# Optimization experiments

Hardware: AMD Instinct MI355X
Metric: run time of the kernel (lower is better)

Reference implementation:

```python
import jax, jax.numpy as jnp
import numpy as np

D_MODEL = 1024
D_KV = 64
N_HEADS = 16
INNER = N_HEADS * D_KV
EPS = 1e-6


def setup_inputs() -> dict:
    key = jax.random.key(0)
    ks = jax.random.split(key, 8)
    B, SQ, SKV = 2, 2048, 4096
    hidden_states = jax.random.normal(ks[0], (B, SQ, D_MODEL), dtype=jnp.float32)
    key_value_states = jax.random.normal(ks[1], (B, SKV, D_MODEL), dtype=jnp.float32)
    attention_mask = jnp.zeros((B, 1, 1, SKV), dtype=jnp.float32)
    # nn.Linear(in, out, bias=False): y = x @ W.T; store W as [in, out] here
    s = 0.02
    Wq = jax.random.normal(ks[2], (D_MODEL, INNER), dtype=jnp.float32) * s
    Wk = jax.random.normal(ks[3], (D_MODEL, INNER), dtype=jnp.float32) * s
    Wv = jax.random.normal(ks[4], (D_MODEL, INNER), dtype=jnp.float32) * s
    Wo = jax.random.normal(ks[5], (INNER, D_MODEL), dtype=jnp.float32) * s
    ln_weight = jnp.ones((D_MODEL,), dtype=jnp.float32)
    return {
        "hidden_states": hidden_states,
        "key_value_states": key_value_states,
        "attention_mask": attention_mask,
        "ln_weight": ln_weight,
        "Wq": Wq,
        "Wk": Wk,
        "Wv": Wv,
        "Wo": Wo,
    }


def _t5_rmsnorm(x, w, eps=EPS):
    # no mean subtraction, variance in fp32
    var = jnp.mean(jnp.square(x.astype(jnp.float32)), axis=-1, keepdims=True)
    return w * (x * jax.lax.rsqrt(var + eps)).astype(x.dtype)


def reference(hidden_states, key_value_states, attention_mask, ln_weight, Wq, Wk, Wv, Wo):
    B, SQ, _ = hidden_states.shape
    SKV = key_value_states.shape[1]
    normed = _t5_rmsnorm(hidden_states, ln_weight)

    # projections -> [B, H, S, Dk]
    q = (normed @ Wq).reshape(B, SQ, N_HEADS, D_KV).transpose(0, 2, 1, 3)
    k = (key_value_states @ Wk).reshape(B, SKV, N_HEADS, D_KV).transpose(0, 2, 1, 3)
    v = (key_value_states @ Wv).reshape(B, SKV, N_HEADS, D_KV).transpose(0, 2, 1, 3)

    # T5: NO 1/sqrt(d) scaling
    scores = jnp.einsum("bhqd,bhkd->bhqk", q, k) + attention_mask
    attn = jax.nn.softmax(scores.astype(jnp.float32), axis=-1).astype(scores.dtype)
    ctx = jnp.einsum("bhqk,bhkd->bhqd", attn, v)
    ctx = ctx.transpose(0, 2, 1, 3).reshape(B, SQ, INNER)
    attn_out = ctx @ Wo
    return hidden_states + attn_out
```

## Files before the change

kernel.cpp:

```cpp
#include <hip/hip_runtime.h>

typedef unsigned short u16;
typedef unsigned int u32;
typedef __attribute__((ext_vector_type(4))) float f32x4;
typedef __attribute__((ext_vector_type(8))) short short8;
typedef __attribute__((ext_vector_type(4))) short short4v;

#define BB   2
#define SQL  2048
#define SKVL 4096
#define DM   1024
#define NH   16
#define DK   64
#define L2E  1.44269504f

#if __has_builtin(__builtin_amdgcn_exp2f)
#define EXP2(x) __builtin_amdgcn_exp2f(x)
#else
#define EXP2(x) exp2f(x)
#endif

#define MFMA32(a, b, c) __builtin_amdgcn_mfma_f32_16x16x32_bf16(a, b, c, 0, 0, 0)

__device__ __forceinline__ u16 f2bf(float f) {
  union { float f; unsigned u; } v; v.f = f;
  unsigned r = v.u + 0x7fff + ((v.u >> 16) & 1);
  return (u16)(r >> 16);
}

__device__ __forceinline__ short4v pack4(float p0, float p1, float p2, float p3) {
  union { float f; u32 u; } a, b, c, d;
  a.f = p0; b.f = p1; c.f = p2; d.f = p3;
  union { uint2 v; short4v s; } r;
  r.v.x = __builtin_amdgcn_perm(b.u + 0x8000u, a.u + 0x8000u, 0x07060302);
  r.v.y = __builtin_amdgcn_perm(d.u + 0x8000u, c.u + 0x8000u, 0x07060302);
  return r.s;
}

__device__ __forceinline__ void gload16(const void* g, void* lds) {
  __builtin_amdgcn_global_load_lds(
      (const __attribute__((address_space(1))) unsigned int*)g,
      (__attribute__((address_space(3))) unsigned int*)lds, 16, 0, 0);
}

__global__ void pre_kernel(const float* __restrict__ hidden, const float* __restrict__ lnw,
                           const float* __restrict__ kvs,
                           const float* __restrict__ Wq, const float* __restrict__ Wk,
                           const float* __restrict__ Wv, const float* __restrict__ Wo,
                           u16* __restrict__ normed, u16* __restrict__ kvb,
                           u16* __restrict__ Wqt, u16* __restrict__ Wkt,
                           u16* __restrict__ Wvt, u16* __restrict__ Wot) {
  __shared__ float red[4];
  __shared__ float tile[32][33];
  int bid = blockIdx.x, t = threadIdx.x;
  if (bid < 4096) {
    int row = bid;
    float4 v = ((const float4*)(hidden + (size_t)row * DM))[t];
    float ss = v.x * v.x + v.y * v.y + v.z * v.z + v.w * v.w;
#pragma unroll
    for (int m = 32; m >= 1; m >>= 1) ss += __shfl_xor(ss, m, 64);
    int lane = t & 63, wv = t >> 6;
    if (lane == 0) red[wv] = ss;
    __syncthreads();
    float total = red[0] + red[1] + red[2] + red[3];
    float scale = rsqrtf(total * (1.0f / DM) + 1e-6f);
    float4 g = ((const float4*)lnw)[t];
    ushort4 o;
    o.x = f2bf(v.x * scale * g.x);
    o.y = f2bf(v.y * scale * g.y);
    o.z = f2bf(v.z * scale * g.z);
    o.w = f2bf(v.w * scale * g.w);
    ((ushort4*)(normed + (size_t)row * DM))[t] = o;
  } else if (bid < 12288) {
    int i = (bid - 4096) * 256 + t;
    float4 v = ((const float4*)kvs)[i];
    ushort4 o;
    o.x = f2bf(v.x); o.y = f2bf(v.y); o.z = f2bf(v.z); o.w = f2bf(v.w);
    ((ushort4*)kvb)[i] = o;
  } else {
    int g = bid - 12288;
    int z = g >> 10;
    const float* W = (z == 0) ? Wq : (z == 1) ? Wk : (z == 2) ? Wv : Wo;
    u16* Wt = (z == 0) ? Wqt : (z == 1) ? Wkt : (z == 2) ? Wvt : Wot;
    int xx = g & 31, yy = (g >> 5) & 31;
    int tx = t & 31, ty = t >> 5;
    int k0 = yy * 32, n0 = xx * 32;
#pragma unroll
    for (int i = 0; i < 4; i++)
      tile[ty + i * 8][tx] = W[(size_t)(k0 + ty + i * 8) * DM + n0 + tx];
    __syncthreads();
#pragma unroll
    for (int i = 0; i < 4; i++)
      Wt[(size_t)(n0 + ty + i * 8) * DM + k0 + tx] = f2bf(tile[tx][ty + i * 8]);
  }
}

__global__ __launch_bounds__(512, 1) void proj_kernel(
    const u16* __restrict__ normed, const u16* __restrict__ kvb,
    const u16* __restrict__ Wqt, const u16* __restrict__ Wkt,
    const u16* __restrict__ Wvt,
    u16* __restrict__ Qb, u16* __restrict__ Kbf, u16* __restrict__ Vtb) {
  const int K = 1024;
  __shared__ __align__(16) u16 Al[256 * 32];
  __shared__ __align__(16) u16 B1[128 * 32];
  __shared__ __align__(16) u16 B2[128 * 32];
  int tid = threadIdx.x, lane = tid & 63, w = tid >> 6;
  int l15 = lane & 15, quad = lane >> 4;
  int wy = w >> 1, wx = w & 1;
  int bid = blockIdx.x;

  if (bid < 256) {
    int tm = (bid >> 3) * 256, tn = (bid & 7) * 128;
    f32x4 ak[4][4] = {}, av[4][4] = {};
    for (int k0 = 0; k0 < K; k0 += 32) {
      __syncthreads();
#pragma unroll
      for (int r = 0; r < 2; r++) {
        int mg = w * 2 + r;
        gload16(kvb + (size_t)(tm + mg * 16 + l15) * K + k0 + quad * 8, &Al[mg * 512]);
      }
      gload16(Wkt + (size_t)(tn + w * 16 + l15) * K + k0 + quad * 8, &B1[w * 512]);
      gload16(Wvt + (size_t)(tn + w * 16 + l15) * K + k0 + quad * 8, &B2[w * 512]);
      __syncthreads();
      short8 af[4], bk[4], bv[4];
#pragma unroll
      for (int i = 0; i < 4; i++) {
        af[i] = *(const short8*)&Al[((wy * 4 + i) * 64 + lane) * 8];
        bk[i] = *(const short8*)&B1[((wx * 4 + i) * 64 + lane) * 8];
        bv[i] = *(const short8*)&B2[((wx * 4 + i) * 64 + lane) * 8];
      }
#pragma unroll
      for (int mt = 0; mt < 4; mt++)
#pragma unroll
        for (int nt = 0; nt < 4; nt++) {
          ak[mt][nt] = MFMA32(af[mt], bk[nt], ak[mt][nt]);
          av[mt][nt] = MFMA32(af[mt], bv[nt], av[mt][nt]);
        }
    }
#pragma unroll
    for (int mt = 0; mt < 4; mt++) {
      int m0 = tm + wy * 64 + mt * 16 + quad * 4;
      int bB = m0 >> 12, skv0 = m0 & 4095;
      int t32 = skv0 >> 5, p0 = skv0 & 31;
#pragma unroll
      for (int nt = 0; nt < 4; nt++) {
        int n = tn + wx * 64 + nt * 16 + l15;
        int h = n >> 6, d0 = n & 63;
        size_t vbase = ((size_t)((bB * NH + h) * 128 + t32)) * 2048
                     + (size_t)(d0 >> 4) * 512 + (size_t)(d0 & 15) * 8;
#pragma unroll
        for (int r = 0; r < 4; r++) {
          Kbf[(size_t)(m0 + r) * 1024 + n] = f2bf(ak[mt][nt][r]);
          int p = p0 + r;
          int s = ((p >> 2) & 3) * 8 + ((p >> 4) & 1) * 4 + (p & 3);
          Vtb[vbase + (s >> 3) * 128 + (s & 7)] = f2bf(av[mt][nt][r]);
        }
      }
    }
  } else {
    int qid = bid - 256;
    int tm = (qid >> 3) * 128, tn = (qid & 7) * 128;
    f32x4 acc[2][4] = {};
    for (int k0 = 0; k0 < K; k0 += 32) {
      __syncthreads();
      gload16(normed + (size_t)(tm + w * 16 + l15) * K + k0 + quad * 8, &Al[w * 512]);
      gload16(Wqt + (size_t)(tn + w * 16 + l15) * K + k0 + quad * 8, &B1[w * 512]);
      __syncthreads();
      short8 af[2], bfr[4];
#pragma unroll
      for (int i = 0; i < 2; i++)
        af[i] = *(const short8*)&Al[((wy * 2 + i) * 64 + lane) * 8];
#pragma unroll
      for (int i = 0; i < 4; i++)
        bfr[i] = *(const short8*)&B1[((wx * 4 + i) * 64 + lane) * 8];
#pragma unroll
      for (int mt = 0; mt < 2; mt++)
#pragma unroll
        for (int nt = 0; nt < 4; nt++)
          acc[mt][nt] = MFMA32(af[mt], bfr[nt], acc[mt][nt]);
    }
#pragma unroll
    for (int mt = 0; mt < 2; mt++) {
      int m0 = tm + wy * 32 + mt * 16 + quad * 4;
#pragma unroll
      for (int nt = 0; nt < 4; nt++) {
        int n = tn + wx * 64 + nt * 16 + l15;
#pragma unroll
        for (int r = 0; r < 4; r++)
          Qb[(size_t)(m0 + r) * 1024 + n] = f2bf(acc[mt][nt][r] * L2E);
      }
    }
  }
}

__global__ __launch_bounds__(256, 2) void flash_kernel(
    const u16* __restrict__ Qp, const u16* __restrict__ Kp, const u16* __restrict__ Vtb,
    const float* __restrict__ mask, u16* __restrict__ ctx) {
  __shared__ __align__(16) char smem[65536];
  u16* Kbuf = (u16*)smem;
  u16* Vbuf = (u16*)(smem + 32768);
  float* Ox = (float*)smem;
  float* Ll = (float*)(smem + 32768);

  int tid = threadIdx.x, lane = tid & 63, w = tid >> 6;
  int l15 = lane & 15, quad = lane >> 4;
  int grp = w >> 1, wg = w & 1;

  int lid = blockIdx.y * 16 + blockIdx.x;
  int xcd = lid & 7, slot = lid >> 3;
  int bh = xcd * 4 + (slot >> 4);
  int qb = slot & 15;
  int b = bh >> 4, h = bh & 15;
  int q0 = qb * 128 + wg * 64;

  short8 qf[4][2];
#pragma unroll
  for (int mt = 0; mt < 4; mt++)
#pragma unroll
    for (int kf = 0; kf < 2; kf++)
      qf[mt][kf] = *(const short8*)(Qp + (size_t)(b * SQL + q0 + mt * 16 + l15) * DM +
                                    h * DK + kf * 32 + quad * 8);

  f32x4 of[4][4] = {};
  f32x4 la[4] = {};
  const short8 ones8 = {0x3F80, 0x3F80, 0x3F80, 0x3F80, 0x3F80, 0x3F80, 0x3F80, 0x3F80};

  const size_t vblob = (size_t)(b * NH + h) * 262144;
  const float* mrow = mask + (size_t)b * SKVL;

  auto stage = [&](int tileIdx, int buf) {
    int kv0 = tileIdx * 64;
    u16* Kd = Kbuf + (buf * 2 + grp) * 4096;
    u16* Vd = Vbuf + (buf * 2 + grp) * 4096;
#pragma unroll
    for (int r = 0; r < 4; r++) {
      int u = wg * 4 + r;
      int kt = u >> 1, kf = u & 1;
      gload16(Kp + (size_t)(b * SKVL + kv0 + kt * 16 + l15) * DM + h * DK + kf * 32 + quad * 8,
              &Kd[u * 512]);
      gload16(Vtb + vblob + (size_t)tileIdx * 4096 + u * 512 + lane * 8, &Vd[u * 512]);
    }
  };

  f32x4 mlc[4], mln[4];
  {
    int kv0 = grp * 64;
#pragma unroll
    for (int kt = 0; kt < 4; kt++)
      mlc[kt] = *(const f32x4*)(mrow + kv0 + kt * 16 + quad * 4) * L2E;
  }
  stage(grp, 0);

  union PU { short8 v8; short4v h2[2]; };

  for (int it = 0; it < 32; ++it) {
    __syncthreads();
    if (it + 1 < 32) {
      stage((it + 1) * 2 + grp, (it + 1) & 1);
      int kvn = ((it + 1) * 2 + grp) * 64;
#pragma unroll
      for (int kt = 0; kt < 4; kt++)
        mln[kt] = *(const f32x4*)(mrow + kvn + kt * 16 + quad * 4) * L2E;
    }
    const u16* Kg = Kbuf + ((it & 1) * 2 + grp) * 4096;
    const u16* Vg = Vbuf + ((it & 1) * 2 + grp) * 4096;

    __builtin_amdgcn_s_setprio(1);
#pragma unroll
    for (int ktp = 0; ktp < 2; ktp++) {
      PU paf[4];
#pragma unroll
      for (int kth = 0; kth < 2; kth++) {
        int kt = ktp * 2 + kth;
        short8 k0 = *(const short8*)&Kg[((kt * 2 + 0) * 64 + lane) * 8];
        short8 k1 = *(const short8*)&Kg[((kt * 2 + 1) * 64 + lane) * 8];
#pragma unroll
        for (int mt = 0; mt < 4; mt++) {
          f32x4 st = mlc[kt];
          st = MFMA32(k0, qf[mt][0], st);
          st = MFMA32(k1, qf[mt][1], st);
          paf[mt].h2[kth] = pack4(EXP2(st[0]), EXP2(st[1]), EXP2(st[2]), EXP2(st[3]));
        }
      }
#pragma unroll
      for (int mt = 0; mt < 4; mt++)
        la[mt] = MFMA32(paf[mt].v8, ones8, la[mt]);
#pragma unroll
      for (int nt = 0; nt < 4; nt++) {
        short8 vv = *(const short8*)&Vg[ktp * 2048 + (nt * 64 + lane) * 8];
#pragma unroll
        for (int mt = 0; mt < 4; mt++)
          of[mt][nt] = MFMA32(paf[mt].v8, vv, of[mt][nt]);
      }
    }
    __builtin_amdgcn_s_setprio(0);
#pragma unroll
    for (int kt = 0; kt < 4; kt++) mlc[kt] = mln[kt];
  }

  __syncthreads();
  if (grp == 1) {
#pragma unroll
    for (int mt = 0; mt < 4; mt++) {
#pragma unroll
      for (int nt = 0; nt < 4; nt++)
#pragma unroll
        for (int r = 0; r < 4; r++)
          Ox[(wg * 64 + mt * 16 + quad * 4 + r) * 64 + nt * 16 + l15] = of[mt][nt][r];
      if (l15 == 0)
#pragma unroll
        for (int r = 0; r < 4; r++) Ll[wg * 64 + mt * 16 + quad * 4 + r] = la[mt][r];
    }
  }
  __syncthreads();
  if (grp == 0) {
#pragma unroll
    for (int mt = 0; mt < 4; mt++)
#pragma unroll
      for (int r = 0; r < 4; r++) {
        int ql = wg * 64 + mt * 16 + quad * 4 + r;
        float inv = 1.0f / (la[mt][r] + Ll[ql]);
        int q = qb * 128 + ql;
#pragma unroll
        for (int nt = 0; nt < 4; nt++) {
          float ov = of[mt][nt][r] + Ox[ql * 64 + nt * 16 + l15];
          ctx[(size_t)(b * SQL + q) * DM + h * DK + nt * 16 + l15] = f2bf(ov * inv);
        }
      }
  }
}

__global__ void ogemm_kernel(const u16* __restrict__ A, const u16* __restrict__ Bt,
                             float* __restrict__ C, const float* __restrict__ resid) {
  const int K = 1024;
  __shared__ __align__(16) u16 Al[128 * 32];
  __shared__ __align__(16) u16 Bl[128 * 32];
  int tid = threadIdx.x, lane = tid & 63, w = tid >> 6;
  int l15 = lane & 15, quad = lane >> 4;
  int wy = w >> 1, wx = w & 1;
  int tm = blockIdx.x * 128, tn = blockIdx.y * 128;
  f32x4 acc[4][4] = {};

  for (int k0 = 0; k0 < K; k0 += 32) {
    __syncthreads();
#pragma unroll
    for (int r = 0; r < 2; r++) {
      int mg = w * 2 + r;
      gload16(A + (size_t)(tm + mg * 16 + l15) * K + k0 + quad * 8, &Al[mg * 512]);
      gload16(Bt + (size_t)(tn + mg * 16 + l15) * K + k0 + quad * 8, &Bl[mg * 512]);
    }
    __syncthreads();
    short8 af[4], bfr[4];
#pragma unroll
    for (int i = 0; i < 4; i++) {
      af[i] = *(const short8*)&Al[((wy * 4 + i) * 64 + lane) * 8];
      bfr[i] = *(const short8*)&Bl[((wx * 4 + i) * 64 + lane) * 8];
    }
#pragma unroll
    for (int mt = 0; mt < 4; mt++)
#pragma unroll
      for (int nt = 0; nt < 4; nt++)
        acc[mt][nt] = MFMA32(af[mt], bfr[nt], acc[mt][nt]);
  }

#pragma unroll
  for (int mt = 0; mt < 4; mt++) {
    int m0 = tm + wy * 64 + mt * 16 + quad * 4;
#pragma unroll
    for (int nt = 0; nt < 4; nt++) {
      int n = tn + wx * 64 + nt * 16 + l15;
#pragma unroll
      for (int r = 0; r < 4; r++) {
        size_t idx = (size_t)(m0 + r) * 1024 + n;
        C[idx] = resid[idx] + acc[mt][nt][r];
      }
    }
  }
}

extern "C" void kernel_launch(void* const* d_in, const int* in_sizes, int n_in,
                              void* d_out, int out_size, void* d_ws, size_t ws_size,
                              hipStream_t stream) {
  const float* hidden = (const float*)d_in[0];
  const float* kvs    = (const float*)d_in[1];
  const float* mask   = (const float*)d_in[2];
  const float* lnw    = (const float*)d_in[3];
  const float* Wq     = (const float*)d_in[4];
  const float* Wk     = (const float*)d_in[5];
  const float* Wv     = (const float*)d_in[6];
  const float* Wo     = (const float*)d_in[7];
  char* ws = (char*)d_ws;

  u16* normed = (u16*)(ws + 0);
  u16* kvb    = (u16*)(ws + 8388608);
  u16* Wqt    = (u16*)(ws + 25165824);
  u16* Wkt    = (u16*)(ws + 27262976);
  u16* Wvt    = (u16*)(ws + 29360128);
  u16* Wot    = (u16*)(ws + 31457280);
  u16* Qb     = (u16*)(ws + 33554432);
  u16* Kbf    = (u16*)(ws + 41943040);
  u16* Vtb    = (u16*)(ws + 58720256);
  u16* ctxb   = (u16*)(ws + 75497472);

  pre_kernel<<<16384, 256, 0, stream>>>(hidden, lnw, kvs, Wq, Wk, Wv, Wo,
                                        normed, kvb, Wqt, Wkt, Wvt, Wot);
  proj_kernel<<<512, 512, 0, stream>>>(normed, kvb, Wqt, Wkt, Wvt, Qb, Kbf, Vtb);
  flash_kernel<<<dim3(SQL / 128, BB * NH), 256, 0, stream>>>(Qb, Kbf, Vtb, mask, ctxb);
  ogemm_kernel<<<dim3(32, 8), 256, 0, stream>>>(ctxb, Wot, (float*)d_out, hidden);
}
```

Measured before the change: 310.4 us.

## Double-buffer LDS in projection GEMM and shrink output GEMM tiles

The projection kernel now keeps two LDS buffers and prefetches the next K-slice while the current one feeds the MFMAs, which removes one barrier per iteration and overlaps global loads with compute. Its launch bounds are raised to allow two blocks per CU. The output GEMM tile shrinks from 128x128 to 64x64, so the grid grows from 256 to 1024 blocks and fills more CUs. The cost is double the LDS use in the projection kernel, possible register pressure from the occupancy hint, and less data reuse per block in the output GEMM.

```diff
diff --git a/kernel.cpp b/kernel.cpp
--- a/kernel.cpp
+++ b/kernel.cpp
@@ -95,15 +95,15 @@
   }
 }
 
-__global__ __launch_bounds__(512, 1) void proj_kernel(
+__global__ __launch_bounds__(512, 2) void proj_kernel(
     const u16* __restrict__ normed, const u16* __restrict__ kvb,
     const u16* __restrict__ Wqt, const u16* __restrict__ Wkt,
     const u16* __restrict__ Wvt,
     u16* __restrict__ Qb, u16* __restrict__ Kbf, u16* __restrict__ Vtb) {
   const int K = 1024;
-  __shared__ __align__(16) u16 Al[256 * 32];
-  __shared__ __align__(16) u16 B1[128 * 32];
-  __shared__ __align__(16) u16 B2[128 * 32];
+  __shared__ __align__(16) u16 Al[2][256 * 32];
+  __shared__ __align__(16) u16 B1[2][128 * 32];
+  __shared__ __align__(16) u16 B2[2][128 * 32];
   int tid = threadIdx.x, lane = tid & 63, w = tid >> 6;
   int l15 = lane & 15, quad = lane >> 4;
   int wy = w >> 1, wx = w & 1;
@@ -112,22 +112,28 @@
   if (bid < 256) {
     int tm = (bid >> 3) * 256, tn = (bid & 7) * 128;
     f32x4 ak[4][4] = {}, av[4][4] = {};
-    for (int k0 = 0; k0 < K; k0 += 32) {
-      __syncthreads();
+
+    auto stage = [&](int k0, int buf) {
 #pragma unroll
       for (int r = 0; r < 2; r++) {
         int mg = w * 2 + r;
-        gload16(kvb + (size_t)(tm + mg * 16 + l15) * K + k0 + quad * 8, &Al[mg * 512]);
-      }
-      gload16(Wkt + (size_t)(tn + w * 16 + l15) * K + k0 + quad * 8, &B1[w * 512]);
-      gload16(Wvt + (size_t)(tn + w * 16 + l15) * K + k0 + quad * 8, &B2[w * 512]);
-      __syncthreads();
+        gload16(kvb + (size_t)(tm + mg * 16 + l15) * K + k0 + quad * 8, &Al[buf][mg * 512]);
+      }
+      gload16(Wkt + (size_t)(tn + w * 16 + l15) * K + k0 + quad * 8, &B1[buf][w * 512]);
+      gload16(Wvt + (size_t)(tn + w * 16 + l15) * K + k0 + quad * 8, &B2[buf][w * 512]);
+    };
+
+    stage(0, 0);
+    __syncthreads();
+    for (int k0 = 0; k0 < K; k0 += 32) {
+      int cur = (k0 >> 5) & 1;
+      if (k0 + 32 < K) stage(k0 + 32, cur ^ 1);
       short8 af[4], bk[4], bv[4];
 #pragma unroll
       for (int i = 0; i < 4; i++) {
-        af[i] = *(const short8*)&Al[((wy * 4 + i) * 64 + lane) * 8];
-        bk[i] = *(const short8*)&B1[((wx * 4 + i) * 64 + lane) * 8];
-        bv[i] = *(const short8*)&B2[((wx * 4 + i) * 64 + lane) * 8];
+        af[i] = *(const short8*)&Al[cur][((wy * 4 + i) * 64 + lane) * 8];
+        bk[i] = *(const short8*)&B1[cur][((wx * 4 + i) * 64 + lane) * 8];
+        bv[i] = *(const short8*)&B2[cur][((wx * 4 + i) * 64 + lane) * 8];
       }
 #pragma unroll
       for (int mt = 0; mt < 4; mt++)
@@ -136,6 +142,7 @@
           ak[mt][nt] = MFMA32(af[mt], bk[nt], ak[mt][nt]);
           av[mt][nt] = MFMA32(af[mt], bv[nt], av[mt][nt]);
         }
+      __syncthreads();
     }
 #pragma unroll
     for (int mt = 0; mt < 4; mt++) {
@@ -161,23 +168,30 @@
     int qid = bid - 256;
     int tm = (qid >> 3) * 128, tn = (qid & 7) * 128;
     f32x4 acc[2][4] = {};
+
+    auto stage = [&](int k0, int buf) {
+      gload16(normed + (size_t)(tm + w * 16 + l15) * K + k0 + quad * 8, &Al[buf][w * 512]);
+      gload16(Wqt + (size_t)(tn + w * 16 + l15) * K + k0 + quad * 8, &B1[buf][w * 512]);
+    };
+
+    stage(0, 0);
+    __syncthreads();
     for (int k0 = 0; k0 < K; k0 += 32) {
-      __syncthreads();
-      gload16(normed + (size_t)(tm + w * 16 + l15) * K + k0 + quad * 8, &Al[w * 512]);
-      gload16(Wqt + (size_t)(tn + w * 16 + l15) * K + k0 + quad * 8, &B1[w * 512]);
-      __syncthreads();
+      int cur = (k0 >> 5) & 1;
+      if (k0 + 32 < K) stage(k0 + 32, cur ^ 1);
       short8 af[2], bfr[4];
 #pragma unroll
       for (int i = 0; i < 2; i++)
-        af[i] = *(const short8*)&Al[((wy * 2 + i) * 64 + lane) * 8];
+        af[i] = *(const short8*)&Al[cur][((wy * 2 + i) * 64 + lane) * 8];
 #pragma unroll
       for (int i = 0; i < 4; i++)
-        bfr[i] = *(const short8*)&B1[((wx * 4 + i) * 64 + lane) * 8];
+        bfr[i] = *(const short8*)&B1[cur][((wx * 4 + i) * 64 + lane) * 8];
 #pragma unroll
       for (int mt = 0; mt < 2; mt++)
 #pragma unroll
         for (int nt = 0; nt < 4; nt++)
           acc[mt][nt] = MFMA32(af[mt], bfr[nt], acc[mt][nt]);
+      __syncthreads();
     }
 #pragma unroll
     for (int mt = 0; mt < 2; mt++) {
@@ -330,45 +344,42 @@
   }
 }
 
-__global__ void ogemm_kernel(const u16* __restrict__ A, const u16* __restrict__ Bt,
-                             float* __restrict__ C, const float* __restrict__ resid) {
+__global__ __launch_bounds__(256) void ogemm_kernel(
+    const u16* __restrict__ A, const u16* __restrict__ Bt,
+    float* __restrict__ C, const float* __restrict__ resid) {
   const int K = 1024;
-  __shared__ __align__(16) u16 Al[128 * 32];
-  __shared__ __align__(16) u16 Bl[128 * 32];
+  __shared__ __align__(16) u16 Al[64 * 32];
+  __shared__ __align__(16) u16 Bl[64 * 32];
   int tid = threadIdx.x, lane = tid & 63, w = tid >> 6;
   int l15 = lane & 15, quad = lane >> 4;
   int wy = w >> 1, wx = w & 1;
-  int tm = blockIdx.x * 128, tn = blockIdx.y * 128;
-  f32x4 acc[4][4] = {};
+  int tm = blockIdx.x * 64, tn = blockIdx.y * 64;
+  f32x4 acc[2][2] = {};
 
   for (int k0 = 0; k0 < K; k0 += 32) {
     __syncthreads();
-#pragma unroll
-    for (int r = 0; r < 2; r++) {
-      int mg = w * 2 + r;
-      gload16(A + (size_t)(tm + mg * 16 + l15) * K + k0 + quad * 8, &Al[mg * 512]);
-      gload16(Bt + (size_t)(tn + mg * 16 + l15) * K + k0 + quad * 8, &Bl[mg * 512]);
-    }
-    __syncthreads();
-    short8 af[4], bfr[4];
-#pragma unroll
-    for (int i = 0; i < 4; i++) {
-      af[i] = *(const short8*)&Al[((wy * 4 + i) * 64 + lane) * 8];
-      bfr[i] = *(const short8*)&Bl[((wx * 4 + i) * 64 + lane) * 8];
-    }
-#pragma unroll
-    for (int mt = 0; mt < 4; mt++)
-#pragma unroll
-      for (int nt = 0; nt < 4; nt++)
+    gload16(A + (size_t)(tm + w * 16 + l15) * K + k0 + quad * 8, &Al[w * 512]);
+    gload16(Bt + (size_t)(tn + w * 16 + l15) * K + k0 + quad * 8, &Bl[w * 512]);
+    __syncthreads();
+    short8 af[2], bfr[2];
+#pragma unroll
+    for (int i = 0; i < 2; i++) {
+      af[i] = *(const short8*)&Al[((wy * 2 + i) * 64 + lane) * 8];
+      bfr[i] = *(const short8*)&Bl[((wx * 2 + i) * 64 + lane) * 8];
+    }
+#pragma unroll
+    for (int mt = 0; mt < 2; mt++)
+#pragma unroll
+      for (int nt = 0; nt < 2; nt++)
         acc[mt][nt] = MFMA32(af[mt], bfr[nt], acc[mt][nt]);
   }
 
 #pragma unroll
-  for (int mt = 0; mt < 4; mt++) {
-    int m0 = tm + wy * 64 + mt * 16 + quad * 4;
-#pragma unroll
-    for (int nt = 0; nt < 4; nt++) {
-      int n = tn + wx * 64 + nt * 16 + l15;
+  for (int mt = 0; mt < 2; mt++) {
+    int m0 = tm + wy * 32 + mt * 16 + quad * 4;
+#pragma unroll
+    for (int nt = 0; nt < 2; nt++) {
+      int n = tn + wx * 32 + nt * 16 + l15;
 #pragma unroll
       for (int r = 0; r < 4; r++) {
         size_t idx = (size_t)(m0 + r) * 1024 + n;
@@ -406,5 +417,5 @@
                                         normed, kvb, Wqt, Wkt, Wvt, Wot);
   proj_kernel<<<512, 512, 0, stream>>>(normed, kvb, Wqt, Wkt, Wvt, Qb, Kbf, Vtb);
   flash_kernel<<<dim3(SQL / 128, BB * NH), 256, 0, stream>>>(Qb, Kbf, Vtb, mask, ctxb);
-  ogemm_kernel<<<dim3(32, 8), 256, 0, stream>>>(ctxb, Wot, (float*)d_out, hidden);
-}
+  ogemm_kernel<<<dim3(64, 16), 256, 0, stream>>>(ctxb, Wot, (float*)d_out, hidden);
+}
```

After: 310.6 us. Within noise of the previous version (+0.1%).

## Double-buffer projection GEMM loads and split flash KV range across four wave groups

Applied to the files above, without the earlier changes.

The projection kernel now double-buffers its LDS tiles so the next K-slice is loaded while the current one feeds MFMAs, with one barrier per iteration instead of two, and requests two blocks per CU. The flash kernel doubles its block to 512 threads, giving four wave groups that each own a contiguous quarter of the KV sequence and process 32-key tiles. Partial outputs and row sums are reduced through LDS in three serial stages. The trade-off is higher LDS and register pressure, which may limit occupancy, plus a longer reduction epilogue.

```diff
diff --git a/kernel.cpp b/kernel.cpp
--- a/kernel.cpp
+++ b/kernel.cpp
@@ -95,15 +95,15 @@
   }
 }
 
-__global__ __launch_bounds__(512, 1) void proj_kernel(
+__global__ __launch_bounds__(512, 2) void proj_kernel(
     const u16* __restrict__ normed, const u16* __restrict__ kvb,
     const u16* __restrict__ Wqt, const u16* __restrict__ Wkt,
     const u16* __restrict__ Wvt,
     u16* __restrict__ Qb, u16* __restrict__ Kbf, u16* __restrict__ Vtb) {
   const int K = 1024;
-  __shared__ __align__(16) u16 Al[256 * 32];
-  __shared__ __align__(16) u16 B1[128 * 32];
-  __shared__ __align__(16) u16 B2[128 * 32];
+  __shared__ __align__(16) u16 Al[2][256 * 32];
+  __shared__ __align__(16) u16 B1[2][128 * 32];
+  __shared__ __align__(16) u16 B2[2][128 * 32];
   int tid = threadIdx.x, lane = tid & 63, w = tid >> 6;
   int l15 = lane & 15, quad = lane >> 4;
   int wy = w >> 1, wx = w & 1;
@@ -112,22 +112,28 @@
   if (bid < 256) {
     int tm = (bid >> 3) * 256, tn = (bid & 7) * 128;
     f32x4 ak[4][4] = {}, av[4][4] = {};
-    for (int k0 = 0; k0 < K; k0 += 32) {
-      __syncthreads();
+
+    auto stage = [&](int k0, int buf) {
 #pragma unroll
       for (int r = 0; r < 2; r++) {
         int mg = w * 2 + r;
-        gload16(kvb + (size_t)(tm + mg * 16 + l15) * K + k0 + quad * 8, &Al[mg * 512]);
-      }
-      gload16(Wkt + (size_t)(tn + w * 16 + l15) * K + k0 + quad * 8, &B1[w * 512]);
-      gload16(Wvt + (size_t)(tn + w * 16 + l15) * K + k0 + quad * 8, &B2[w * 512]);
-      __syncthreads();
+        gload16(kvb + (size_t)(tm + mg * 16 + l15) * K + k0 + quad * 8, &Al[buf][mg * 512]);
+      }
+      gload16(Wkt + (size_t)(tn + w * 16 + l15) * K + k0 + quad * 8, &B1[buf][w * 512]);
+      gload16(Wvt + (size_t)(tn + w * 16 + l15) * K + k0 + quad * 8, &B2[buf][w * 512]);
+    };
+
+    stage(0, 0);
+    __syncthreads();
+    for (int k0 = 0; k0 < K; k0 += 32) {
+      int cur = (k0 >> 5) & 1;
+      if (k0 + 32 < K) stage(k0 + 32, cur ^ 1);
       short8 af[4], bk[4], bv[4];
 #pragma unroll
       for (int i = 0; i < 4; i++) {
-        af[i] = *(const short8*)&Al[((wy * 4 + i) * 64 + lane) * 8];
-        bk[i] = *(const short8*)&B1[((wx * 4 + i) * 64 + lane) * 8];
-        bv[i] = *(const short8*)&B2[((wx * 4 + i) * 64 + lane) * 8];
+        af[i] = *(const short8*)&Al[cur][((wy * 4 + i) * 64 + lane) * 8];
+        bk[i] = *(const short8*)&B1[cur][((wx * 4 + i) * 64 + lane) * 8];
+        bv[i] = *(const short8*)&B2[cur][((wx * 4 + i) * 64 + lane) * 8];
       }
 #pragma unroll
       for (int mt = 0; mt < 4; mt++)
@@ -136,6 +142,7 @@
           ak[mt][nt] = MFMA32(af[mt], bk[nt], ak[mt][nt]);
           av[mt][nt] = MFMA32(af[mt], bv[nt], av[mt][nt]);
         }
+      __syncthreads();
     }
 #pragma unroll
     for (int mt = 0; mt < 4; mt++) {
@@ -161,23 +168,30 @@
     int qid = bid - 256;
     int tm = (qid >> 3) * 128, tn = (qid & 7) * 128;
     f32x4 acc[2][4] = {};
+
+    auto stage = [&](int k0, int buf) {
+      gload16(normed + (size_t)(tm + w * 16 + l15) * K + k0 + quad * 8, &Al[buf][w * 512]);
+      gload16(Wqt + (size_t)(tn + w * 16 + l15) * K + k0 + quad * 8, &B1[buf][w * 512]);
+    };
+
+    stage(0, 0);
+    __syncthreads();
     for (int k0 = 0; k0 < K; k0 += 32) {
-      __syncthreads();
-      gload16(normed + (size_t)(tm + w * 16 + l15) * K + k0 + quad * 8, &Al[w * 512]);
-      gload16(Wqt + (size_t)(tn + w * 16 + l15) * K + k0 + quad * 8, &B1[w * 512]);
-      __syncthreads();
+      int cur = (k0 >> 5) & 1;
+      if (k0 + 32 < K) stage(k0 + 32, cur ^ 1);
       short8 af[2], bfr[4];
 #pragma unroll
       for (int i = 0; i < 2; i++)
-        af[i] = *(const short8*)&Al[((wy * 2 + i) * 64 + lane) * 8];
+        af[i] = *(const short8*)&Al[cur][((wy * 2 + i) * 64 + lane) * 8];
 #pragma unroll
       for (int i = 0; i < 4; i++)
-        bfr[i] = *(const short8*)&B1[((wx * 4 + i) * 64 + lane) * 8];
+        bfr[i] = *(const short8*)&B1[cur][((wx * 4 + i) * 64 + lane) * 8];
 #pragma unroll
       for (int mt = 0; mt < 2; mt++)
 #pragma unroll
         for (int nt = 0; nt < 4; nt++)
           acc[mt][nt] = MFMA32(af[mt], bfr[nt], acc[mt][nt]);
+      __syncthreads();
     }
 #pragma unroll
     for (int mt = 0; mt < 2; mt++) {
@@ -193,7 +207,7 @@
   }
 }
 
-__global__ __launch_bounds__(256, 2) void flash_kernel(
+__global__ __launch_bounds__(512, 2) void flash_kernel(
     const u16* __restrict__ Qp, const u16* __restrict__ Kp, const u16* __restrict__ Vtb,
     const float* __restrict__ mask, u16* __restrict__ ctx) {
   __shared__ __align__(16) char smem[65536];
@@ -228,78 +242,71 @@
   const size_t vblob = (size_t)(b * NH + h) * 262144;
   const float* mrow = mask + (size_t)b * SKVL;
 
-  auto stage = [&](int tileIdx, int buf) {
-    int kv0 = tileIdx * 64;
-    u16* Kd = Kbuf + (buf * 2 + grp) * 4096;
-    u16* Vd = Vbuf + (buf * 2 + grp) * 4096;
-#pragma unroll
-    for (int r = 0; r < 4; r++) {
-      int u = wg * 4 + r;
-      int kt = u >> 1, kf = u & 1;
-      gload16(Kp + (size_t)(b * SKVL + kv0 + kt * 16 + l15) * DM + h * DK + kf * 32 + quad * 8,
-              &Kd[u * 512]);
-      gload16(Vtb + vblob + (size_t)tileIdx * 4096 + u * 512 + lane * 8, &Vd[u * 512]);
+  auto stage = [&](int it, int buf) {
+    int t32 = grp * 32 + it;
+    u16* Kd = Kbuf + (grp * 2 + buf) * 2048;
+    u16* Vd = Vbuf + (grp * 2 + buf) * 2048;
+#pragma unroll
+    for (int r = 0; r < 2; r++) {
+      int c = wg * 2 + r;
+      int kt = c >> 1, kf = c & 1;
+      gload16(Kp + (size_t)(b * SKVL + t32 * 32 + kt * 16 + l15) * DM + h * DK + kf * 32 + quad * 8,
+              &Kd[c * 512]);
+      gload16(Vtb + vblob + (size_t)t32 * 2048 + c * 512 + lane * 8, &Vd[c * 512]);
     }
   };
 
-  f32x4 mlc[4], mln[4];
-  {
-    int kv0 = grp * 64;
-#pragma unroll
-    for (int kt = 0; kt < 4; kt++)
-      mlc[kt] = *(const f32x4*)(mrow + kv0 + kt * 16 + quad * 4) * L2E;
-  }
-  stage(grp, 0);
+  f32x4 mlc[2], mln[2];
+#pragma unroll
+  for (int kt = 0; kt < 2; kt++)
+    mlc[kt] = *(const f32x4*)(mrow + grp * 1024 + kt * 16 + quad * 4) * L2E;
+  stage(0, 0);
 
   union PU { short8 v8; short4v h2[2]; };
 
   for (int it = 0; it < 32; ++it) {
     __syncthreads();
     if (it + 1 < 32) {
-      stage((it + 1) * 2 + grp, (it + 1) & 1);
-      int kvn = ((it + 1) * 2 + grp) * 64;
-#pragma unroll
-      for (int kt = 0; kt < 4; kt++)
+      stage(it + 1, (it + 1) & 1);
+      int kvn = (grp * 32 + it + 1) * 32;
+#pragma unroll
+      for (int kt = 0; kt < 2; kt++)
         mln[kt] = *(const f32x4*)(mrow + kvn + kt * 16 + quad * 4) * L2E;
     }
-    const u16* Kg = Kbuf + ((it & 1) * 2 + grp) * 4096;
-    const u16* Vg = Vbuf + ((it & 1) * 2 + grp) * 4096;
+    const u16* Kg = Kbuf + (grp * 2 + (it & 1)) * 2048;
+    const u16* Vg = Vbuf + (grp * 2 + (it & 1)) * 2048;
 
     __builtin_amdgcn_s_setprio(1);
-#pragma unroll
-    for (int ktp = 0; ktp < 2; ktp++) {
-      PU paf[4];
-#pragma unroll
-      for (int kth = 0; kth < 2; kth++) {
-        int kt = ktp * 2 + kth;
-        short8 k0 = *(const short8*)&Kg[((kt * 2 + 0) * 64 + lane) * 8];
-        short8 k1 = *(const short8*)&Kg[((kt * 2 + 1) * 64 + lane) * 8];
-#pragma unroll
-        for (int mt = 0; mt < 4; mt++) {
-          f32x4 st = mlc[kt];
-          st = MFMA32(k0, qf[mt][0], st);
-          st = MFMA32(k1, qf[mt][1], st);
-          paf[mt].h2[kth] = pack4(EXP2(st[0]), EXP2(st[1]), EXP2(st[2]), EXP2(st[3]));
-        }
-      }
+    PU paf[4];
+#pragma unroll
+    for (int kt = 0; kt < 2; kt++) {
+      short8 k0 = *(const short8*)&Kg[((kt * 2 + 0) * 64 + lane) * 8];
+      short8 k1 = *(const short8*)&Kg[((kt * 2 + 1) * 64 + lane) * 8];
+#pragma unroll
+      for (int mt = 0; mt < 4; mt++) {
+        f32x4 st = mlc[kt];
+        st = MFMA32(k0, qf[mt][0], st);
+        st = MFMA32(k1, qf[mt][1], st);
+        paf[mt].h2[kt] = pack4(EXP2(st[0]), EXP2(st[1]), EXP2(st[2]), EXP2(st[3]));
+      }
+    }
+#pragma unroll
+    for (int mt = 0; mt < 4; mt++)
+      la[mt] = MFMA32(paf[mt].v8, ones8, la[mt]);
+#pragma unroll
+    for (int nt = 0; nt < 4; nt++) {
+      short8 vv = *(const short8*)&Vg[(nt * 64 + lane) * 8];
 #pragma unroll
       for (int mt = 0; mt < 4; mt++)
-        la[mt] = MFMA32(paf[mt].v8, ones8, la[mt]);
-#pragma unroll
-      for (int nt = 0; nt < 4; nt++) {
-        short8 vv = *(const short8*)&Vg[ktp * 2048 + (nt * 64 + lane) * 8];
-#pragma unroll
-        for (int mt = 0; mt < 4; mt++)
-          of[mt][nt] = MFMA32(paf[mt].v8, vv, of[mt][nt]);
-      }
+        of[mt][nt] = MFMA32(paf[mt].v8, vv, of[mt][nt]);
     }
     __builtin_amdgcn_s_setprio(0);
 #pragma unroll
-    for (int kt = 0; kt < 4; kt++) mlc[kt] = mln[kt];
+    for (int kt = 0; kt < 2; kt++) mlc[kt] = mln[kt];
   }
 
   __syncthreads();
-  if (grp == 1) {
+  if (grp == 3) {
 #pragma unroll
     for (int mt = 0; mt < 4; mt++) {
 #pragma unroll
@@ -310,6 +317,34 @@
       if (l15 == 0)
 #pragma unroll
         for (int r = 0; r < 4; r++) Ll[wg * 64 + mt * 16 + quad * 4 + r] = la[mt][r];
+    }
+  }
+  __syncthreads();
+  if (grp == 2) {
+#pragma unroll
+    for (int mt = 0; mt < 4; mt++) {
+#pragma unroll
+      for (int nt = 0; nt < 4; nt++)
+#pragma unroll
+        for (int r = 0; r < 4; r++)
+          Ox[(wg * 64 + mt * 16 + quad * 4 + r) * 64 + nt * 16 + l15] += of[mt][nt][r];
+      if (l15 == 0)
+#pragma unroll
+        for (int r = 0; r < 4; r++) Ll[wg * 64 + mt * 16 + quad * 4 + r] += la[mt][r];
+    }
+  }
+  __syncthreads();
+  if (grp == 1) {
+#pragma unroll
+    for (int mt = 0; mt < 4; mt++) {
+#pragma unroll
+      for (int nt = 0; nt < 4; nt++)
+#pragma unroll
+        for (int r = 0; r < 4; r++)
+          Ox[(wg * 64 + mt * 16 + quad * 4 + r) * 64 + nt * 16 + l15] += of[mt][nt][r];
+      if (l15 == 0)
+#pragma unroll
+        for (int r = 0; r < 4; r++) Ll[wg * 64 + mt * 16 + quad * 4 + r] += la[mt][r];
     }
   }
   __syncthreads();
@@ -405,6 +440,6 @@
   pre_kernel<<<16384, 256, 0, stream>>>(hidden, lnw, kvs, Wq, Wk, Wv, Wo,
                                         normed, kvb, Wqt, Wkt, Wvt, Wot);
   proj_kernel<<<512, 512, 0, stream>>>(normed, kvb, Wqt, Wkt, Wvt, Qb, Kbf, Vtb);
-  flash_kernel<<<dim3(SQL / 128, BB * NH), 256, 0, stream>>>(Qb, Kbf, Vtb, mask, ctxb);
+  flash_kernel<<<dim3(SQL / 128, BB * NH), 512, 0, stream>>>(Qb, Kbf, Vtb, mask, ctxb);
   ogemm_kernel<<<dim3(32, 8), 256, 0, stream>>>(ctxb, Wot, (float*)d_out, hidden);
 }
```

Result: slower. 348.0 us (+12.1%).

## Double-buffer LDS tiles in projection GEMM and reorder tile mapping

Applied to the files above, without the earlier changes.

Splits the projection kernel's shared-memory tiles into two buffers so the next K-slice is loaded while the MFMAs run on the current one, leaving one barrier per iteration instead of two. It also swaps the block-to-tile mapping so that consecutive blocks walk along M while sharing the same weight columns, which should improve L2 reuse of the weight tiles. The launch bound is raised to request two blocks per CU. The cost is twice the LDS footprint (64 KB) and higher register pressure under the tighter occupancy bound, which may cause spills.

```diff
diff --git a/kernel.cpp b/kernel.cpp
--- a/kernel.cpp
+++ b/kernel.cpp
@@ -95,39 +95,45 @@
   }
 }
 
-__global__ __launch_bounds__(512, 1) void proj_kernel(
+__global__ __launch_bounds__(512, 2) void proj_kernel(
     const u16* __restrict__ normed, const u16* __restrict__ kvb,
     const u16* __restrict__ Wqt, const u16* __restrict__ Wkt,
     const u16* __restrict__ Wvt,
     u16* __restrict__ Qb, u16* __restrict__ Kbf, u16* __restrict__ Vtb) {
   const int K = 1024;
-  __shared__ __align__(16) u16 Al[256 * 32];
-  __shared__ __align__(16) u16 B1[128 * 32];
-  __shared__ __align__(16) u16 B2[128 * 32];
+  __shared__ __align__(16) u16 Al[2][256 * 32];
+  __shared__ __align__(16) u16 B1[2][128 * 32];
+  __shared__ __align__(16) u16 B2[2][128 * 32];
   int tid = threadIdx.x, lane = tid & 63, w = tid >> 6;
   int l15 = lane & 15, quad = lane >> 4;
   int wy = w >> 1, wx = w & 1;
   int bid = blockIdx.x;
 
   if (bid < 256) {
-    int tm = (bid >> 3) * 256, tn = (bid & 7) * 128;
+    int tm = (bid & 31) * 256, tn = (bid >> 5) * 128;
     f32x4 ak[4][4] = {}, av[4][4] = {};
-    for (int k0 = 0; k0 < K; k0 += 32) {
-      __syncthreads();
+
+    auto stage = [&](int k0, int buf) {
 #pragma unroll
       for (int r = 0; r < 2; r++) {
         int mg = w * 2 + r;
-        gload16(kvb + (size_t)(tm + mg * 16 + l15) * K + k0 + quad * 8, &Al[mg * 512]);
-      }
-      gload16(Wkt + (size_t)(tn + w * 16 + l15) * K + k0 + quad * 8, &B1[w * 512]);
-      gload16(Wvt + (size_t)(tn + w * 16 + l15) * K + k0 + quad * 8, &B2[w * 512]);
-      __syncthreads();
+        gload16(kvb + (size_t)(tm + mg * 16 + l15) * K + k0 + quad * 8, &Al[buf][mg * 512]);
+      }
+      gload16(Wkt + (size_t)(tn + w * 16 + l15) * K + k0 + quad * 8, &B1[buf][w * 512]);
+      gload16(Wvt + (size_t)(tn + w * 16 + l15) * K + k0 + quad * 8, &B2[buf][w * 512]);
+    };
+
+    stage(0, 0);
+    __syncthreads();
+    for (int k0 = 0; k0 < K; k0 += 32) {
+      int cur = (k0 >> 5) & 1;
+      if (k0 + 32 < K) stage(k0 + 32, cur ^ 1);
       short8 af[4], bk[4], bv[4];
 #pragma unroll
       for (int i = 0; i < 4; i++) {
-        af[i] = *(const short8*)&Al[((wy * 4 + i) * 64 + lane) * 8];
-        bk[i] = *(const short8*)&B1[((wx * 4 + i) * 64 + lane) * 8];
-        bv[i] = *(const short8*)&B2[((wx * 4 + i) * 64 + lane) * 8];
+        af[i] = *(const short8*)&Al[cur][((wy * 4 + i) * 64 + lane) * 8];
+        bk[i] = *(const short8*)&B1[cur][((wx * 4 + i) * 64 + lane) * 8];
+        bv[i] = *(const short8*)&B2[cur][((wx * 4 + i) * 64 + lane) * 8];
       }
 #pragma unroll
       for (int mt = 0; mt < 4; mt++)
@@ -136,6 +142,7 @@
           ak[mt][nt] = MFMA32(af[mt], bk[nt], ak[mt][nt]);
           av[mt][nt] = MFMA32(af[mt], bv[nt], av[mt][nt]);
         }
+      __syncthreads();
     }
 #pragma unroll
     for (int mt = 0; mt < 4; mt++) {
@@ -159,25 +166,32 @@
     }
   } else {
     int qid = bid - 256;
-    int tm = (qid >> 3) * 128, tn = (qid & 7) * 128;
+    int tm = (qid & 31) * 128, tn = (qid >> 5) * 128;
     f32x4 acc[2][4] = {};
+
+    auto stage = [&](int k0, int buf) {
+      gload16(normed + (size_t)(tm + w * 16 + l15) * K + k0 + quad * 8, &Al[buf][w * 512]);
+      gload16(Wqt + (size_t)(tn + w * 16 + l15) * K + k0 + quad * 8, &B1[buf][w * 512]);
+    };
+
+    stage(0, 0);
+    __syncthreads();
     for (int k0 = 0; k0 < K; k0 += 32) {
-      __syncthreads();
-      gload16(normed + (size_t)(tm + w * 16 + l15) * K + k0 + quad * 8, &Al[w * 512]);
-      gload16(Wqt + (size_t)(tn + w * 16 + l15) * K + k0 + quad * 8, &B1[w * 512]);
-      __syncthreads();
+      int cur = (k0 >> 5) & 1;
+      if (k0 + 32 < K) stage(k0 + 32, cur ^ 1);
       short8 af[2], bfr[4];
 #pragma unroll
       for (int i = 0; i < 2; i++)
-        af[i] = *(const short8*)&Al[((wy * 2 + i) * 64 + lane) * 8];
+        af[i] = *(const short8*)&Al[cur][((wy * 2 + i) * 64 + lane) * 8];
 #pragma unroll
       for (int i = 0; i < 4; i++)
-        bfr[i] = *(const short8*)&B1[((wx * 4 + i) * 64 + lane) * 8];
+        bfr[i] = *(const short8*)&B1[cur][((wx * 4 + i) * 64 + lane) * 8];
 #pragma unroll
       for (int mt = 0; mt < 2; mt++)
 #pragma unroll
         for (int nt = 0; nt < 4; nt++)
           acc[mt][nt] = MFMA32(af[mt], bfr[nt], acc[mt][nt]);
+      __syncthreads();
     }
 #pragma unroll
     for (int mt = 0; mt < 2; mt++) {
```

Result: faster. 303.3 us (-2.3%).
